# Kernel optimization log

Hardware: AMD Instinct MI355X
Metric: run time of the kernel (lower is better)

## Reference

```python
import jax, jax.numpy as jnp
import numpy as np

N = 500_000
E = 8_000_000
IN, HID, OUT = 1, 10, 4
BN_EPS = 1e-5


def _lin_init(key, fan_in, fan_out):
    kw, kb = jax.random.split(key)
    s = 1.0 / np.sqrt(fan_in)
    W = jax.random.uniform(kw, (fan_in, fan_out), minval=-s, maxval=s, dtype=jnp.float32)
    b = jax.random.uniform(kb, (fan_out,), minval=-s, maxval=s, dtype=jnp.float32)
    return W, b


def setup_inputs() -> dict:
    key = jax.random.key(0)
    ks = jax.random.split(key, 12)
    x = jax.random.normal(ks[0], (N, IN), dtype=jnp.float32)
    edge_index = jax.random.randint(ks[1], (2, E), 0, N, dtype=jnp.int64)
    edge_attr = jax.random.uniform(ks[2], (E,), dtype=jnp.float32)
    inp = {"x": x, "edge_index": edge_index, "edge_attr": edge_attr}
    dims = [(IN, HID), (HID, HID), (HID, HID)]
    for i, (di, do) in enumerate(dims, start=1):
        k1, k2 = jax.random.split(ks[2 + i])
        W1, b1 = _lin_init(k1, di, do)
        W2, b2 = _lin_init(k2, do, do)
        inp[f"W{i}a"], inp[f"b{i}a"] = W1, b1
        inp[f"W{i}b"], inp[f"b{i}b"] = W2, b2
        inp[f"g{i}"] = jnp.ones((do,), jnp.float32)
        inp[f"be{i}"] = jnp.zeros((do,), jnp.float32)
    Wf, bf = _lin_init(ks[10], 3 * HID, OUT)
    inp["Wf"], inp["bf"] = Wf, bf
    return inp


def _gin_layer(x, src, dst, Wa, ba, Wb, bb, g, be):
    # GINConv (eps=0): h_i = MLP(x_i + sum_{j->i} x_j); Linear->Linear->BatchNorm (train mode)
    agg = jax.ops.segment_sum(x[src], dst, num_segments=N)  # [N, d]
    h = x + agg
    h = h @ Wa + ba
    h = h @ Wb + bb
    mu = jnp.mean(h, axis=0)
    var = jnp.var(h, axis=0)
    return g * (h - mu) * jax.lax.rsqrt(var + BN_EPS) + be


def _modularity(s, src, dst, w):
    two_m = jnp.sum(w)
    pos = jnp.sum(w * jnp.sum(s[src] * s[dst], axis=-1)) / two_m
    deg = jax.ops.segment_sum(w, src, num_segments=N)  # [N]
    ds = (deg @ s) / two_m  # [OUT]
    return pos - jnp.sum(ds * ds)


def reference(x, edge_index, edge_attr,
              W1a, b1a, W1b, b1b, g1, be1,
              W2a, b2a, W2b, b2b, g2, be2,
              W3a, b3a, W3b, b3b, g3, be3,
              Wf, bf):
    src, dst = edge_index[0], edge_index[1]
    x11 = _gin_layer(x, src, dst, W1a, b1a, W1b, b1b, g1, be1)
    x12 = _gin_layer(x11, src, dst, W2a, b2a, W2b, b2b, g2, be2)
    x13 = _gin_layer(x12, src, dst, W3a, b3a, W3b, b3b, g3, be3)
    logits = jnp.concatenate([x11, x12, x13], axis=-1) @ Wf + bf
    s = jax.nn.softmax(logits, axis=-1)
    q = _modularity(s, src, dst, edge_attr)
    return s, q
```

## Files before the change

### kernel.cpp

```cpp
#include <hip/hip_runtime.h>
#include <hip/hip_bf16.h>

#define NN 500000
#define NE 8000000
#define NB 123
#define BSH 12
#define BSZ 4096
#define CAP 69632
#define M 8
#define NAGG (NB * M)
#define BN_EPS 1e-5f

typedef unsigned uv4 __attribute__((ext_vector_type(4)));
typedef int iv4 __attribute__((ext_vector_type(4)));
typedef float fv4 __attribute__((ext_vector_type(4)));
typedef unsigned long long u64;

__device__ __forceinline__ float waveReduceF(float v) {
#pragma unroll
    for (int o = 32; o > 0; o >>= 1) v += __shfl_down(v, o, 64);
    return v;
}
__device__ __forceinline__ double waveReduceD(double v) {
#pragma unroll
    for (int o = 32; o > 0; o >>= 1) v += __shfl_down(v, o, 64);
    return v;
}
__device__ __forceinline__ float u2f(unsigned short u) {
    return __bfloat162float(__builtin_bit_cast(__hip_bfloat16, u));
}
__device__ __forceinline__ unsigned short f2u(float f) {
    return __builtin_bit_cast(unsigned short, __float2bfloat16(f));
}
__device__ __forceinline__ u64 pk1(float v) {
    int iv = (int)rintf(v * 268435456.f);
    return ((u64)(long long)iv << 20) + 1ull;
}

__global__ __launch_bounds__(512) void scatterk(
    const iv4* __restrict__ src4, const iv4* __restrict__ dst4,
    const fv4* __restrict__ w4, int* __restrict__ cur,
    unsigned* __restrict__ pairs, unsigned short* __restrict__ wp)
{
    __shared__ unsigned sEnt[4096];
    __shared__ unsigned short sW[4096];
    __shared__ unsigned char sB[4096];
    __shared__ int h[8][128];
    __shared__ int wOff[8][128];
    __shared__ int bOff[128];
    __shared__ int lb[128];
    __shared__ int tot[128];

    int tid = threadIdx.x, wv = tid >> 6;
    for (int j = tid; j < 8 * 128; j += 512) (&h[0][0])[j] = 0;
    __syncthreads();

    unsigned en[8]; unsigned short wb[8]; int rb[8];
#pragma unroll
    for (int k = 0; k < 2; k++) {
        int q = blockIdx.x * 1024 + k * 512 + tid;
        if (q < NE / 4) {
            iv4 s4 = __builtin_nontemporal_load(src4 + q);
            iv4 d4 = __builtin_nontemporal_load(dst4 + q);
            fv4 ww = __builtin_nontemporal_load(w4 + q);
            int ss[4] = {s4.x, s4.y, s4.z, s4.w};
            int dd[4] = {d4.x, d4.y, d4.z, d4.w};
            float fw[4] = {ww.x, ww.y, ww.z, ww.w};
#pragma unroll
            for (int i = 0; i < 4; i++) {
                int d = dd[i], b = d >> BSH;
                en[k * 4 + i] = ((unsigned)(d & (BSZ - 1)) << 19) | (unsigned)ss[i];
                wb[k * 4 + i] = f2u(fw[i]);
                int rk = atomicAdd(&h[wv][b], 1);
                rb[k * 4 + i] = (rk << 8) | b;
            }
        } else {
#pragma unroll
            for (int i = 0; i < 4; i++) rb[k * 4 + i] = -1;
        }
    }
    __syncthreads();
    if (tid < NB) {
        int acc = 0;
#pragma unroll
        for (int w = 0; w < 8; w++) { wOff[w][tid] = acc; acc += h[w][tid]; }
        tot[tid] = acc;
        lb[tid] = tid * CAP + atomicAdd(&cur[tid], acc);
    }
    __syncthreads();
    if (tid < 64) {
        int lane = tid;
        int a = (2 * lane < NB) ? tot[2 * lane] : 0;
        int b = (2 * lane + 1 < NB) ? tot[2 * lane + 1] : 0;
        int s = a + b;
#pragma unroll
        for (int o = 1; o < 64; o <<= 1) {
            int t = __shfl_up(s, o, 64);
            if (lane >= o) s += t;
        }
        int excl = s - (a + b);
        bOff[2 * lane] = excl;
        bOff[2 * lane + 1] = excl + a;
    }
    __syncthreads();
#pragma unroll
    for (int k = 0; k < 8; k++) {
        if (rb[k] >= 0) {
            int b = rb[k] & 255, rk = rb[k] >> 8;
            int pos = bOff[b] + wOff[wv][b] + rk;
            sEnt[pos] = en[k]; sW[pos] = wb[k]; sB[pos] = (unsigned char)b;
        }
    }
    __syncthreads();
    int nE = NE - blockIdx.x * 4096; if (nE > 4096) nE = 4096;
    for (int j = tid; j < nE; j += 512) {
        int b = sB[j];
        int glob = lb[b] + (j - bOff[b]);
        __builtin_nontemporal_store(sEnt[j], pairs + glob);
        __builtin_nontemporal_store(sW[j], wp + glob);
    }
}

__global__ __launch_bounds__(512) void agg1k(
    const unsigned* __restrict__ pairs, const int* __restrict__ cur,
    const float* __restrict__ x, u64* __restrict__ slab)
{
    __shared__ u64 t[BSZ];
    for (int j = threadIdx.x; j < BSZ; j += 512) t[j] = 0ull;
    __syncthreads();
    int B = blockIdx.x / M, sl = blockIdx.x % M;
    int b0 = B * CAP;
    int len = cur[B];
    int seg = (((len + M - 1) / M) + 3) & ~3;
    int lo = b0 + sl * seg;
    int hi = lo + seg, e1 = b0 + len;
    if (hi > e1) hi = e1;
    int n = hi - lo;
    if (n > 0) {
        int nq = n >> 2;
        const uv4* pq = (const uv4*)(pairs + lo);
        for (int i = threadIdx.x; i < nq; i += 1024) {
            uv4 pA = __builtin_nontemporal_load(pq + i);
            int iB = i + 512;
            bool vB = iB < nq;
            float a0 = x[pA.x & 524287u];
            float a1 = x[pA.y & 524287u];
            float a2 = x[pA.z & 524287u];
            float a3 = x[pA.w & 524287u];
            float c0, c1, c2, c3; unsigned d4, d5, d6, d7;
            if (vB) {
                uv4 pB = __builtin_nontemporal_load(pq + iB);
                c0 = x[pB.x & 524287u]; d4 = pB.x >> 19;
                c1 = x[pB.y & 524287u]; d5 = pB.y >> 19;
                c2 = x[pB.z & 524287u]; d6 = pB.z >> 19;
                c3 = x[pB.w & 524287u]; d7 = pB.w >> 19;
            }
            atomicAdd(&t[pA.x >> 19], pk1(a0));
            atomicAdd(&t[pA.y >> 19], pk1(a1));
            atomicAdd(&t[pA.z >> 19], pk1(a2));
            atomicAdd(&t[pA.w >> 19], pk1(a3));
            if (vB) {
                atomicAdd(&t[d4], pk1(c0));
                atomicAdd(&t[d5], pk1(c1));
                atomicAdd(&t[d6], pk1(c2));
                atomicAdd(&t[d7], pk1(c3));
            }
        }
        int rem = n & 3;
        if ((int)threadIdx.x < rem) {
            unsigned p = pairs[lo + (nq << 2) + threadIdx.x];
            atomicAdd(&t[p >> 19], pk1(x[p & 524287u]));
        }
    }
    __syncthreads();
    u64* sb = slab + (size_t)blockIdx.x * BSZ;
    for (int j = threadIdx.x; j < BSZ; j += 512)
        __builtin_nontemporal_store(t[j], sb + j);
}

__global__ __launch_bounds__(256) void mergeN1(
    const u64* __restrict__ slab, const float* __restrict__ x,
    float2* __restrict__ UN2, u64* __restrict__ ENC)
{
    int i = blockIdx.x * 256 + threadIdx.x;
    if (i >= NN) return;
    int B = i >> BSH, low = i & (BSZ - 1);
    u64 s = 0ull;
#pragma unroll
    for (int m = 0; m < M; m++)
        s += __builtin_nontemporal_load(slab + (size_t)(B * M + m) * BSZ + low);
    unsigned cn = (unsigned)(s & 0xFFFFFull);
    long long sv = (long long)(s - (u64)cn) >> 20;
    float u = x[i] + (float)((double)sv * 3.725290298461914e-09);
    UN2[i] = make_float2(u, (float)cn);
    long long iu = (long long)rintf(u * 67108864.f);
    ENC[i] = ((u64)iu << 22) + (u64)cn;
}

__global__ __launch_bounds__(512) void agg2k(
    const unsigned* __restrict__ pairs, const int* __restrict__ cur,
    const u64* __restrict__ ENC, u64* __restrict__ slab)
{
    __shared__ u64 t[BSZ];
    for (int j = threadIdx.x; j < BSZ; j += 512) t[j] = 0ull;
    __syncthreads();
    int B = blockIdx.x / M, sl = blockIdx.x % M;
    int b0 = B * CAP;
    int len = cur[B];
    int seg = (((len + M - 1) / M) + 3) & ~3;
    int lo = b0 + sl * seg;
    int hi = lo + seg, e1 = b0 + len;
    if (hi > e1) hi = e1;
    int n = hi - lo;
    if (n > 0) {
        int nq = n >> 2;
        const uv4* pq = (const uv4*)(pairs + lo);
        for (int i = threadIdx.x; i < nq; i += 1024) {
            uv4 pA = __builtin_nontemporal_load(pq + i);
            int iB = i + 512;
            bool vB = iB < nq;
            u64 e0 = ENC[pA.x & 524287u];
            u64 e1v = ENC[pA.y & 524287u];
            u64 e2 = ENC[pA.z & 524287u];
            u64 e3 = ENC[pA.w & 524287u];
            u64 e4, e5, e6, e7; unsigned d4, d5, d6, d7;
            if (vB) {
                uv4 pB = __builtin_nontemporal_load(pq + iB);
                e4 = ENC[pB.x & 524287u]; d4 = pB.x >> 19;
                e5 = ENC[pB.y & 524287u]; d5 = pB.y >> 19;
                e6 = ENC[pB.z & 524287u]; d6 = pB.z >> 19;
                e7 = ENC[pB.w & 524287u]; d7 = pB.w >> 19;
            }
            atomicAdd(&t[pA.x >> 19], e0);
            atomicAdd(&t[pA.y >> 19], e1v);
            atomicAdd(&t[pA.z >> 19], e2);
            atomicAdd(&t[pA.w >> 19], e3);
            if (vB) {
                atomicAdd(&t[d4], e4);
                atomicAdd(&t[d5], e5);
                atomicAdd(&t[d6], e6);
                atomicAdd(&t[d7], e7);
            }
        }
        int rem = n & 3;
        if ((int)threadIdx.x < rem) {
            unsigned p = pairs[lo + (nq << 2) + threadIdx.x];
            atomicAdd(&t[p >> 19], ENC[p & 524287u]);
        }
    }
    __syncthreads();
    u64* sb = slab + (size_t)blockIdx.x * BSZ;
    for (int j = threadIdx.x; j < BSZ; j += 512)
        __builtin_nontemporal_store(t[j], sb + j);
}

__global__ __launch_bounds__(256) void mergeN2(
    const u64* __restrict__ slab, float* __restrict__ SU, float* __restrict__ SN)
{
    int i = blockIdx.x * 256 + threadIdx.x;
    if (i >= NN) return;
    int B = i >> BSH, low = i & (BSZ - 1);
    u64 s = 0ull;
#pragma unroll
    for (int m = 0; m < M; m++)
        s += __builtin_nontemporal_load(slab + (size_t)(B * M + m) * BSZ + low);
    unsigned sn = (unsigned)(s & 0x3FFFFFull);
    long long sv = (long long)(s - (u64)sn) >> 22;
    float su = (float)((double)sv * 1.4901161193847656e-08);
    SU[i] = su;
    SN[i] = (float)sn;
}

__global__ __launch_bounds__(512) void agg3k(
    const unsigned* __restrict__ pairs, const int* __restrict__ cur,
    const float* __restrict__ SU, float* __restrict__ slab)
{
    __shared__ float t[BSZ];
    for (int j = threadIdx.x; j < BSZ; j += 512) t[j] = 0.f;
    __syncthreads();
    int B = blockIdx.x / M, sl = blockIdx.x % M;
    int b0 = B * CAP;
    int len = cur[B];
    int seg = (((len + M - 1) / M) + 3) & ~3;
    int lo = b0 + sl * seg;
    int hi = lo + seg, e1 = b0 + len;
    if (hi > e1) hi = e1;
    int n = hi - lo;
    if (n > 0) {
        int nq = n >> 2;
        const uv4* pq = (const uv4*)(pairs + lo);
        for (int i = threadIdx.x; i < nq; i += 1024) {
            uv4 pA = __builtin_nontemporal_load(pq + i);
            int iB = i + 512;
            bool vB = iB < nq;
            float a0 = SU[pA.x & 524287u];
            float a1 = SU[pA.y & 524287u];
            float a2 = SU[pA.z & 524287u];
            float a3 = SU[pA.w & 524287u];
            float c0, c1, c2, c3; unsigned d4, d5, d6, d7;
            if (vB) {
                uv4 pB = __builtin_nontemporal_load(pq + iB);
                c0 = SU[pB.x & 524287u]; d4 = pB.x >> 19;
                c1 = SU[pB.y & 524287u]; d5 = pB.y >> 19;
                c2 = SU[pB.z & 524287u]; d6 = pB.z >> 19;
                c3 = SU[pB.w & 524287u]; d7 = pB.w >> 19;
            }
            atomicAdd(&t[pA.x >> 19], a0);
            atomicAdd(&t[pA.y >> 19], a1);
            atomicAdd(&t[pA.z >> 19], a2);
            atomicAdd(&t[pA.w >> 19], a3);
            if (vB) {
                atomicAdd(&t[d4], c0);
                atomicAdd(&t[d5], c1);
                atomicAdd(&t[d6], c2);
                atomicAdd(&t[d7], c3);
            }
        }
        int rem = n & 3;
        if ((int)threadIdx.x < rem) {
            unsigned p = pairs[lo + (nq << 2) + threadIdx.x];
            atomicAdd(&t[p >> 19], SU[p & 524287u]);
        }
    }
    __syncthreads();
    float* sb = slab + (size_t)blockIdx.x * BSZ;
    for (int j = threadIdx.x; j < BSZ; j += 512)
        __builtin_nontemporal_store(t[j], sb + j);
}

__global__ __launch_bounds__(256) void m3mom(
    const float* __restrict__ slab, const float2* __restrict__ UN2,
    const float* __restrict__ SU, const float* __restrict__ SN,
    float* __restrict__ SSU, double* __restrict__ dm)
{
    int i = blockIdx.x * 256 + threadIdx.x;
    double z[5] = {0, 0, 0, 0, 0};
    if (i < NN) {
        int B = i >> BSH, low = i & (BSZ - 1);
        float ssu = 0.f;
#pragma unroll
        for (int m = 0; m < M; m++)
            ssu += __builtin_nontemporal_load(slab + (size_t)(B * M + m) * BSZ + low);
        SSU[i] = ssu;
        float2 un = UN2[i];
        z[0] = (double)un.x; z[1] = (double)un.y; z[2] = (double)SU[i];
        z[3] = (double)SN[i]; z[4] = (double)ssu;
    }
    double m[20];
#pragma unroll
    for (int a = 0; a < 5; a++) m[a] = z[a];
    int idx = 5;
#pragma unroll
    for (int a = 0; a < 5; a++)
#pragma unroll
        for (int b = a; b < 5; b++) m[idx++] = z[a] * z[b];

    __shared__ double part[4][20];
    int lane = threadIdx.x & 63, wid = threadIdx.x >> 6;
#pragma unroll
    for (int k = 0; k < 20; k++) {
        double r = waveReduceD(m[k]);
        if (lane == 0) part[wid][k] = r;
    }
    __syncthreads();
    if (threadIdx.x < 20)
        atomicAdd(&dm[threadIdx.x],
                  part[0][threadIdx.x] + part[1][threadIdx.x] +
                  part[2][threadIdx.x] + part[3][threadIdx.x]);
}

__global__ __launch_bounds__(64) void constk(
    const float* __restrict__ W1a, const float* __restrict__ b1a,
    const float* __restrict__ W1b, const float* __restrict__ b1b,
    const float* __restrict__ g1, const float* __restrict__ be1,
    const float* __restrict__ W2a, const float* __restrict__ b2a,
    const float* __restrict__ W2b, const float* __restrict__ b2b,
    const float* __restrict__ g2, const float* __restrict__ be2,
    const float* __restrict__ W3a, const float* __restrict__ b3a,
    const float* __restrict__ W3b, const float* __restrict__ b3b,
    const float* __restrict__ g3, const float* __restrict__ be3,
    const float* __restrict__ Wf, const float* __restrict__ bf_,
    const double* __restrict__ dm, float* __restrict__ Lout)
{
    __shared__ float sw[768];
    __shared__ double sdm[20];
    __shared__ float vv[9][10];
    int t = threadIdx.x;
    if (t < 10) {
        sw[0 + t] = W1a[t];  sw[10 + t] = b1a[t];  sw[120 + t] = b1b[t];
        sw[130 + t] = g1[t]; sw[140 + t] = be1[t];
        sw[250 + t] = b2a[t]; sw[360 + t] = b2b[t];
        sw[370 + t] = g2[t]; sw[380 + t] = be2[t];
        sw[490 + t] = b3a[t]; sw[600 + t] = b3b[t];
        sw[610 + t] = g3[t]; sw[620 + t] = be3[t];
    }
    for (int i = t; i < 100; i += 64) {
        sw[20 + i]  = W1b[i];
        sw[150 + i] = W2a[i];
        sw[260 + i] = W2b[i];
        sw[390 + i] = W3a[i];
        sw[500 + i] = W3b[i];
    }
    for (int i = t; i < 120; i += 64) sw[630 + i] = Wf[i];
    if (t < 4)  sw[750 + t] = bf_[t];
    if (t < 20) sdm[t] = dm[t];
    __syncthreads();

    const double invN = 1.0 / (double)NN;
    double E[5];
#pragma unroll
    for (int m = 0; m < 5; m++) E[m] = sdm[m] * invN;
    double C[5][5];
    {
        int idx = 5;
#pragma unroll
        for (int a = 0; a < 5; a++)
#pragma unroll
            for (int b = a; b < 5; b++) {
                double c = sdm[idx++] * invN - E[a] * E[b];
                C[a][b] = c; C[b][a] = c;
            }
    }
    int j = t;
    if (j < 10) {
        float vj = 0.f;
        for (int k = 0; k < 10; k++) vj += sw[0 + k] * sw[20 + k * 10 + j];
        float var1 = (float)(C[0][0] * (double)vj * (double)vj);
        float sc1 = sw[130 + j] * rsqrtf(var1 + BN_EPS);
        float pj = sc1 * vj;
        float qj = sw[140 + j] - (float)E[0] * pj;
        vv[0][j] = pj; vv[1][j] = qj;
    }
    __syncthreads();
    if (j < 10) {
        float tp[10], tq[10];
        for (int m = 0; m < 10; m++) {
            float ap = 0.f, aq = 0.f;
            for (int k = 0; k < 10; k++) {
                float w = sw[150 + k * 10 + m];
                ap += vv[0][k] * w; aq += vv[1][k] * w;
            }
            tp[m] = ap; tq[m] = aq;
        }
        float rj = 0.f, sj = 0.f;
        for (int m = 0; m < 10; m++) {
            float w = sw[260 + m * 10 + j];
            rj += tp[m] * w; sj += tq[m] * w;
        }
        double Ea = E[0] + E[2], Eb = 1.0 + E[1];
        double Va = C[0][0] + 2.0 * C[0][2] + C[2][2];
        double Vb = C[1][1];
        double Cab = C[0][1] + C[2][1];
        double rjd = rj, sjd = sj;
        float var2 = (float)(Va * rjd * rjd + Vb * sjd * sjd + 2.0 * Cab * rjd * sjd);
        float sc2 = sw[370 + j] * rsqrtf(var2 + BN_EPS);
        vv[2][j] = sc2 * rj;
        vv[3][j] = sc2 * sj;
        vv[4][j] = sw[380 + j] - sc2 * (float)(Ea * rjd + Eb * sjd);
    }
    __syncthreads();
    if (j < 10) {
        float tr[10], ts[10], tt[10];
        for (int m = 0; m < 10; m++) {
            float ar = 0.f, as = 0.f, at = 0.f;
            for (int k = 0; k < 10; k++) {
                float w = sw[390 + k * 10 + m];
                ar += vv[2][k] * w; as += vv[3][k] * w; at += vv[4][k] * w;
            }
            tr[m] = ar; ts[m] = as; tt[m] = at;
        }
        float r3 = 0.f, s3 = 0.f, t3 = 0.f;
        for (int m = 0; m < 10; m++) {
            float w = sw[500 + m * 10 + j];
            r3 += tr[m] * w; s3 += ts[m] * w; t3 += tt[m] * w;
        }
        const double gA[5] = {1, 0, 2, 0, 1};
        const double gB[5] = {0, 2, 0, 1, 0};
        const double gC[5] = {0, 1, 0, 0, 0};
        double EA = E[0] + 2.0 * E[2] + E[4];
        double EB = 1.0 + 2.0 * E[1] + E[3];
        double EC = 1.0 + E[1];
        double VA = 0, VB = 0, VC = 0, CAB = 0, CAC = 0, CBC = 0;
        for (int a = 0; a < 5; a++)
            for (int b = 0; b < 5; b++) {
                double c = C[a][b];
                VA  += gA[a] * gA[b] * c;
                VB  += gB[a] * gB[b] * c;
                VC  += gC[a] * gC[b] * c;
                CAB += gA[a] * gB[b] * c;
                CAC += gA[a] * gC[b] * c;
                CBC += gB[a] * gC[b] * c;
            }
        double r3d = r3, s3d = s3, t3d = t3;
        float var3 = (float)(VA * r3d * r3d + VB * s3d * s3d + VC * t3d * t3d
                             + 2.0 * (CAB * r3d * s3d + CAC * r3d * t3d + CBC * s3d * t3d));
        float sc3 = sw[610 + j] * rsqrtf(var3 + BN_EPS);
        vv[5][j] = sc3 * r3;
        vv[6][j] = sc3 * s3;
        vv[7][j] = sc3 * t3;
        vv[8][j] = sw[620 + j] - sc3 * (float)(EA * r3d + EB * s3d + EC * t3d);
    }
    __syncthreads();
    if (t < 4) {
        int k = t;
        float Lu = 0, Ln = 0, Lsu = 0, Lsn = 0, Lssu = 0, L0 = sw[750 + k];
        for (int j2 = 0; j2 < 10; j2++) {
            float wf1 = sw[630 + j2 * 4 + k];
            float wf2 = sw[630 + (10 + j2) * 4 + k];
            float wf3 = sw[630 + (20 + j2) * 4 + k];
            Lu   += vv[0][j2] * wf1 + vv[2][j2] * wf2 + vv[5][j2] * wf3;
            Ln   += vv[3][j2] * wf2 + (2.f * vv[6][j2] + vv[7][j2]) * wf3;
            Lsu  += vv[2][j2] * wf2 + 2.f * vv[5][j2] * wf3;
            Lsn  += vv[6][j2] * wf3;
            Lssu += vv[5][j2] * wf3;
            L0   += vv[1][j2] * wf1 + (vv[3][j2] + vv[4][j2]) * wf2
                  + (vv[6][j2] + vv[7][j2] + vv[8][j2]) * wf3;
        }
        Lout[0 * 4 + k] = Lu;  Lout[1 * 4 + k] = Ln;   Lout[2 * 4 + k] = Lsu;
        Lout[3 * 4 + k] = Lsn; Lout[4 * 4 + k] = Lssu; Lout[5 * 4 + k] = L0;
    }
}

__global__ __launch_bounds__(256) void finalk(
    const float2* __restrict__ UN2, const float* __restrict__ SU,
    const float* __restrict__ SN, const float* __restrict__ SSU,
    const float* __restrict__ L,
    float4* __restrict__ sout, ushort4* __restrict__ sbf)
{
    __shared__ float sL[24];
    if (threadIdx.x < 24) sL[threadIdx.x] = L[threadIdx.x];
    __syncthreads();
    int i = blockIdx.x * 256 + threadIdx.x;
    if (i >= NN) return;
    float2 un = UN2[i];
    float u = un.x, n = un.y, su = SU[i], sn = SN[i], ssu = SSU[i];
    float lg[4];
#pragma unroll
    for (int k = 0; k < 4; k++)
        lg[k] = sL[k] * u + sL[4 + k] * n + sL[8 + k] * su
              + sL[12 + k] * sn + sL[16 + k] * ssu + sL[20 + k];
    float mx = fmaxf(fmaxf(lg[0], lg[1]), fmaxf(lg[2], lg[3]));
    float e0 = __expf(lg[0] - mx), e1 = __expf(lg[1] - mx);
    float e2 = __expf(lg[2] - mx), e3 = __expf(lg[3] - mx);
    float inv = 1.f / (e0 + e1 + e2 + e3);
    float s0 = e0 * inv, s1 = e1 * inv, s2 = e2 * inv, s3 = e3 * inv;
    fv4 o = {s0, s1, s2, s3};
    __builtin_nontemporal_store(o, (fv4*)sout + i);
    ushort4 pk; pk.x = f2u(s0); pk.y = f2u(s1); pk.z = f2u(s2); pk.w = f2u(s3);
    sbf[i] = pk;
}

__device__ __forceinline__ void modacc(u64 ua, u64 ub, float we, float* acc) {
    float ax = u2f((unsigned short)ua),         ay = u2f((unsigned short)(ua >> 16));
    float az = u2f((unsigned short)(ua >> 32)), aw = u2f((unsigned short)(ua >> 48));
    float bx = u2f((unsigned short)ub),         by = u2f((unsigned short)(ub >> 16));
    float bz = u2f((unsigned short)(ub >> 32)), bw = u2f((unsigned short)(ub >> 48));
    acc[0] += we;
    acc[1] += we * (ax * bx + ay * by + az * bz + aw * bw);
    acc[2] += we * ax; acc[3] += we * ay;
    acc[4] += we * az; acc[5] += we * aw;
}

__global__ __launch_bounds__(512) void modk(
    const unsigned* __restrict__ pairs, const unsigned short* __restrict__ wp,
    const int* __restrict__ cur, const u64* __restrict__ sbfU,
    float* __restrict__ scal)
{
    __shared__ u64 sS[BSZ];
    int B = blockIdx.x / M, sl = blockIdx.x % M;
    for (int j = threadIdx.x; j < BSZ; j += 512) {
        int g = (B << BSH) + j;
        sS[j] = (g < NN) ? sbfU[g] : 0ull;
    }
    __syncthreads();
    int b0 = B * CAP;
    int len = cur[B];
    int seg = (((len + M - 1) / M) + 3) & ~3;
    int lo = b0 + sl * seg;
    int hi = lo + seg, e1 = b0 + len;
    if (hi > e1) hi = e1;
    int n = hi - lo;
    float acc[6] = {0, 0, 0, 0, 0, 0};
    if (n > 0) {
        int nq = n >> 2;
        const uv4* pq = (const uv4*)(pairs + lo);
        const u64* wq = (const u64*)(wp + lo);
        for (int i = threadIdx.x; i < nq; i += 1024) {
            uv4 pA = __builtin_nontemporal_load(pq + i);
            u64 wA = __builtin_nontemporal_load(wq + i);
            int iB = i + 512;
            bool vB = iB < nq;
            u64 a0 = sbfU[pA.x & 524287u];
            u64 a1 = sbfU[pA.y & 524287u];
            u64 a2 = sbfU[pA.z & 524287u];
            u64 a3 = sbfU[pA.w & 524287u];
            uv4 pB; u64 wB; u64 a4, a5, a6, a7;
            if (vB) {
                pB = __builtin_nontemporal_load(pq + iB);
                wB = __builtin_nontemporal_load(wq + iB);
                a4 = sbfU[pB.x & 524287u];
                a5 = sbfU[pB.y & 524287u];
                a6 = sbfU[pB.z & 524287u];
                a7 = sbfU[pB.w & 524287u];
            }
            modacc(a0, sS[pA.x >> 19], u2f((unsigned short)wA),         acc);
            modacc(a1, sS[pA.y >> 19], u2f((unsigned short)(wA >> 16)), acc);
            modacc(a2, sS[pA.z >> 19], u2f((unsigned short)(wA >> 32)), acc);
            modacc(a3, sS[pA.w >> 19], u2f((unsigned short)(wA >> 48)), acc);
            if (vB) {
                modacc(a4, sS[pB.x >> 19], u2f((unsigned short)wB),         acc);
                modacc(a5, sS[pB.y >> 19], u2f((unsigned short)(wB >> 16)), acc);
                modacc(a6, sS[pB.z >> 19], u2f((unsigned short)(wB >> 32)), acc);
                modacc(a7, sS[pB.w >> 19], u2f((unsigned short)(wB >> 48)), acc);
            }
        }
        int rem = n & 3;
        if ((int)threadIdx.x < rem) {
            int idx = lo + (nq << 2) + threadIdx.x;
            unsigned p = pairs[idx];
            modacc(sbfU[p & 524287u], sS[p >> 19], u2f(wp[idx]), acc);
        }
    }
    __shared__ float part[8][6];
    int lane = threadIdx.x & 63, wid = threadIdx.x >> 6;
#pragma unroll
    for (int k = 0; k < 6; k++) {
        float r = waveReduceF(acc[k]);
        if (lane == 0) part[wid][k] = r;
    }
    __syncthreads();
    if (threadIdx.x < 6) {
        float vsum = 0.f;
#pragma unroll
        for (int wdi = 0; wdi < 8; wdi++) vsum += part[wdi][threadIdx.x];
        int off = (threadIdx.x == 0) ? 128 : (threadIdx.x == 1 ? 129 : 130 + threadIdx.x);
        atomicAdd(&scal[off], vsum);
    }
}

__global__ void qk(const float* __restrict__ scal, float* __restrict__ out)
{
    if (threadIdx.x == 0) {
        float inv = 1.f / scal[128];
        float posv = scal[129] * inv;
        float acc = 0.f;
#pragma unroll
        for (int k = 0; k < 4; k++) {
            float d = scal[132 + k] * inv;
            acc += d * d;
        }
        out[(size_t)NN * 4] = posv - acc;
    }
}

extern "C" void kernel_launch(void* const* d_in, const int* in_sizes, int n_in,
                              void* d_out, int out_size, void* d_ws, size_t ws_size,
                              hipStream_t stream) {
    const float* x  = (const float*)d_in[0];
    const int*  ei  = (const int*)d_in[1];
    const int*  src = ei;
    const int*  dst = ei + NE;
    const float* w   = (const float*)d_in[2];
    const float* W1a = (const float*)d_in[3];  const float* b1a = (const float*)d_in[4];
    const float* W1b = (const float*)d_in[5];  const float* b1b = (const float*)d_in[6];
    const float* g1  = (const float*)d_in[7];  const float* be1 = (const float*)d_in[8];
    const float* W2a = (const float*)d_in[9];  const float* b2a = (const float*)d_in[10];
    const float* W2b = (const float*)d_in[11]; const float* b2b = (const float*)d_in[12];
    const float* g2  = (const float*)d_in[13]; const float* be2 = (const float*)d_in[14];
    const float* W3a = (const float*)d_in[15]; const float* b3a = (const float*)d_in[16];
    const float* W3b = (const float*)d_in[17]; const float* b3b = (const float*)d_in[18];
    const float* g3  = (const float*)d_in[19]; const float* be3 = (const float*)d_in[20];
    const float* Wf  = (const float*)d_in[21]; const float* bfb = (const float*)d_in[22];

    float*  sc   = (float*)d_ws;
    int*    sci  = (int*)d_ws;
    double* dm   = (double*)(sc + 384);
    unsigned* pairs = (unsigned*)(sc + 1024);
    unsigned short* wp = (unsigned short*)(pairs + (size_t)NB * CAP);
    float*  slab = (float*)(wp + (size_t)NB * CAP);
    u64*    slabU = (u64*)slab;
    float2* UN2  = (float2*)(slab + (size_t)NAGG * 2 * BSZ);
    float*  SU   = (float*)(UN2 + NN);
    float*  SN   = SU + NN;
    float*  SSU  = SN + NN;
    ushort4* sbf = (ushort4*)(SSU + NN);
    u64*    ENC  = (u64*)(sbf + NN);
    float*  sout = (float*)d_out;

    const int NB_N  = (NN + 255) / 256;
    const int NB_EQ = (NE / 4 + 1023) / 1024;

    hipMemsetAsync(sc, 0, 4096, stream);

    scatterk<<<NB_EQ, 512, 0, stream>>>((const iv4*)src, (const iv4*)dst,
                                        (const fv4*)w, sci + 832, pairs, wp);

    agg1k<<<NAGG, 512, 0, stream>>>(pairs, sci + 832, x, slabU);
    mergeN1<<<NB_N, 256, 0, stream>>>(slabU, x, UN2, ENC);
    agg2k<<<NAGG, 512, 0, stream>>>(pairs, sci + 832, ENC, slabU);
    mergeN2<<<NB_N, 256, 0, stream>>>(slabU, SU, SN);
    agg3k<<<NAGG, 512, 0, stream>>>(pairs, sci + 832, SU, slab);
    m3mom<<<NB_N, 256, 0, stream>>>(slab, UN2, SU, SN, SSU, dm);

    constk<<<1, 64, 0, stream>>>(W1a, b1a, W1b, b1b, g1, be1,
                                 W2a, b2a, W2b, b2b, g2, be2,
                                 W3a, b3a, W3b, b3b, g3, be3,
                                 Wf, bfb, dm, sc + 160);

    finalk<<<NB_N, 256, 0, stream>>>(UN2, SU, SN, SSU, sc + 160, (float4*)sout, sbf);
    modk<<<NAGG, 512, 0, stream>>>(pairs, wp, sci + 832, (const u64*)sbf, sc);
    qk<<<1, 64, 0, stream>>>(sc, sout);
}
```

Baseline: 480.5 us.

## Software-pipeline gather loops with rotating prefetch and simplify scatter bucketing

The three aggregation kernels now keep three iterations of index and gathered-value loads in flight ahead of the shared-memory atomics. The modularity kernel keeps one iteration of lookahead. This is meant to hide global gather latency behind the LDS atomics, at the cost of more live registers and possibly lower occupancy. The scatter kernel also drops its per-wave histograms for a single block-wide histogram and packs entry, weight and bucket into one 64-bit shared array. That removes a prefix pass and a barrier, but it makes the in-bucket order nondeterministic and puts all eight waves' atomics on the same counters.

```diff
diff --git a/kernel.cpp b/kernel.cpp
--- a/kernel.cpp
+++ b/kernel.cpp
@@ -10,6 +10,7 @@
 #define M 8
 #define NAGG (NB * M)
 #define BN_EPS 1e-5f
+#define M19 524287u
 
 typedef unsigned uv4 __attribute__((ext_vector_type(4)));
 typedef int iv4 __attribute__((ext_vector_type(4)));
@@ -42,17 +43,13 @@
     const fv4* __restrict__ w4, int* __restrict__ cur,
     unsigned* __restrict__ pairs, unsigned short* __restrict__ wp)
 {
-    __shared__ unsigned sEnt[4096];
-    __shared__ unsigned short sW[4096];
-    __shared__ unsigned char sB[4096];
-    __shared__ int h[8][128];
-    __shared__ int wOff[8][128];
+    __shared__ u64 sPack[4096];
+    __shared__ int h[128];
     __shared__ int bOff[128];
     __shared__ int lb[128];
-    __shared__ int tot[128];
-
-    int tid = threadIdx.x, wv = tid >> 6;
-    for (int j = tid; j < 8 * 128; j += 512) (&h[0][0])[j] = 0;
+
+    int tid = threadIdx.x;
+    for (int j = tid; j < 128; j += 512) h[j] = 0;
     __syncthreads();
 
     unsigned en[8]; unsigned short wb[8]; int rb[8];
@@ -71,7 +68,7 @@
                 int d = dd[i], b = d >> BSH;
                 en[k * 4 + i] = ((unsigned)(d & (BSZ - 1)) << 19) | (unsigned)ss[i];
                 wb[k * 4 + i] = f2u(fw[i]);
-                int rk = atomicAdd(&h[wv][b], 1);
+                int rk = atomicAdd(&h[b], 1);
                 rb[k * 4 + i] = (rk << 8) | b;
             }
         } else {
@@ -80,18 +77,11 @@
         }
     }
     __syncthreads();
-    if (tid < NB) {
-        int acc = 0;
-#pragma unroll
-        for (int w = 0; w < 8; w++) { wOff[w][tid] = acc; acc += h[w][tid]; }
-        tot[tid] = acc;
-        lb[tid] = tid * CAP + atomicAdd(&cur[tid], acc);
-    }
-    __syncthreads();
+    if (tid < NB) lb[tid] = tid * CAP + atomicAdd(&cur[tid], h[tid]);
     if (tid < 64) {
         int lane = tid;
-        int a = (2 * lane < NB) ? tot[2 * lane] : 0;
-        int b = (2 * lane + 1 < NB) ? tot[2 * lane + 1] : 0;
+        int a = (2 * lane < NB) ? h[2 * lane] : 0;
+        int b = (2 * lane + 1 < NB) ? h[2 * lane + 1] : 0;
         int s = a + b;
 #pragma unroll
         for (int o = 1; o < 64; o <<= 1) {
@@ -107,17 +97,18 @@
     for (int k = 0; k < 8; k++) {
         if (rb[k] >= 0) {
             int b = rb[k] & 255, rk = rb[k] >> 8;
-            int pos = bOff[b] + wOff[wv][b] + rk;
-            sEnt[pos] = en[k]; sW[pos] = wb[k]; sB[pos] = (unsigned char)b;
+            int pos = bOff[b] + rk;
+            sPack[pos] = ((u64)en[k] << 32) | ((u64)wb[k] << 16) | (unsigned)b;
         }
     }
     __syncthreads();
     int nE = NE - blockIdx.x * 4096; if (nE > 4096) nE = 4096;
     for (int j = tid; j < nE; j += 512) {
-        int b = sB[j];
+        u64 v = sPack[j];
+        int b = (int)(v & 0xFF);
         int glob = lb[b] + (j - bOff[b]);
-        __builtin_nontemporal_store(sEnt[j], pairs + glob);
-        __builtin_nontemporal_store(sW[j], wp + glob);
+        __builtin_nontemporal_store((unsigned)(v >> 32), pairs + glob);
+        __builtin_nontemporal_store((unsigned short)(v >> 16), wp + glob);
     }
 }
 
@@ -139,37 +130,48 @@
     if (n > 0) {
         int nq = n >> 2;
         const uv4* pq = (const uv4*)(pairs + lo);
-        for (int i = threadIdx.x; i < nq; i += 1024) {
-            uv4 pA = __builtin_nontemporal_load(pq + i);
-            int iB = i + 512;
-            bool vB = iB < nq;
-            float a0 = x[pA.x & 524287u];
-            float a1 = x[pA.y & 524287u];
-            float a2 = x[pA.z & 524287u];
-            float a3 = x[pA.w & 524287u];
-            float c0, c1, c2, c3; unsigned d4, d5, d6, d7;
-            if (vB) {
-                uv4 pB = __builtin_nontemporal_load(pq + iB);
-                c0 = x[pB.x & 524287u]; d4 = pB.x >> 19;
-                c1 = x[pB.y & 524287u]; d5 = pB.y >> 19;
-                c2 = x[pB.z & 524287u]; d6 = pB.z >> 19;
-                c3 = x[pB.w & 524287u]; d7 = pB.w >> 19;
+        int i1 = threadIdx.x;
+        uv4 pA; float a0, a1, a2, a3; bool vA = i1 < nq;
+        if (vA) {
+            pA = __builtin_nontemporal_load(pq + i1);
+            a0 = x[pA.x & M19]; a1 = x[pA.y & M19];
+            a2 = x[pA.z & M19]; a3 = x[pA.w & M19];
+        }
+        int i2 = i1 + 512;
+        uv4 pB; float b0v, b1v, b2v, b3v; bool vB = i2 < nq;
+        if (vB) {
+            pB = __builtin_nontemporal_load(pq + i2);
+            b0v = x[pB.x & M19]; b1v = x[pB.y & M19];
+            b2v = x[pB.z & M19]; b3v = x[pB.w & M19];
+        }
+        int i3 = i2 + 512;
+        uv4 pC; float c0, c1, c2, c3; bool vC = i3 < nq;
+        if (vC) {
+            pC = __builtin_nontemporal_load(pq + i3);
+            c0 = x[pC.x & M19]; c1 = x[pC.y & M19];
+            c2 = x[pC.z & M19]; c3 = x[pC.w & M19];
+        }
+        int inx = i3 + 512;
+        while (vA) {
+            uv4 pD; float d0, d1, d2, d3; bool vD = inx < nq;
+            if (vD) {
+                pD = __builtin_nontemporal_load(pq + inx);
+                d0 = x[pD.x & M19]; d1 = x[pD.y & M19];
+                d2 = x[pD.z & M19]; d3 = x[pD.w & M19];
             }
             atomicAdd(&t[pA.x >> 19], pk1(a0));
             atomicAdd(&t[pA.y >> 19], pk1(a1));
             atomicAdd(&t[pA.z >> 19], pk1(a2));
             atomicAdd(&t[pA.w >> 19], pk1(a3));
-            if (vB) {
-                atomicAdd(&t[d4], pk1(c0));
-                atomicAdd(&t[d5], pk1(c1));
-                atomicAdd(&t[d6], pk1(c2));
-                atomicAdd(&t[d7], pk1(c3));
-            }
+            pA = pB; a0 = b0v; a1 = b1v; a2 = b2v; a3 = b3v; vA = vB;
+            pB = pC; b0v = c0; b1v = c1; b2v = c2; b3v = c3; vB = vC;
+            pC = pD; c0 = d0; c1 = d1; c2 = d2; c3 = d3; vC = vD;
+            inx += 512;
         }
         int rem = n & 3;
         if ((int)threadIdx.x < rem) {
             unsigned p = pairs[lo + (nq << 2) + threadIdx.x];
-            atomicAdd(&t[p >> 19], pk1(x[p & 524287u]));
+            atomicAdd(&t[p >> 19], pk1(x[p & M19]));
         }
     }
     __syncthreads();
@@ -215,37 +217,48 @@
     if (n > 0) {
         int nq = n >> 2;
         const uv4* pq = (const uv4*)(pairs + lo);
-        for (int i = threadIdx.x; i < nq; i += 1024) {
-            uv4 pA = __builtin_nontemporal_load(pq + i);
-            int iB = i + 512;
-            bool vB = iB < nq;
-            u64 e0 = ENC[pA.x & 524287u];
-            u64 e1v = ENC[pA.y & 524287u];
-            u64 e2 = ENC[pA.z & 524287u];
-            u64 e3 = ENC[pA.w & 524287u];
-            u64 e4, e5, e6, e7; unsigned d4, d5, d6, d7;
-            if (vB) {
-                uv4 pB = __builtin_nontemporal_load(pq + iB);
-                e4 = ENC[pB.x & 524287u]; d4 = pB.x >> 19;
-                e5 = ENC[pB.y & 524287u]; d5 = pB.y >> 19;
-                e6 = ENC[pB.z & 524287u]; d6 = pB.z >> 19;
-                e7 = ENC[pB.w & 524287u]; d7 = pB.w >> 19;
-            }
-            atomicAdd(&t[pA.x >> 19], e0);
-            atomicAdd(&t[pA.y >> 19], e1v);
-            atomicAdd(&t[pA.z >> 19], e2);
-            atomicAdd(&t[pA.w >> 19], e3);
-            if (vB) {
-                atomicAdd(&t[d4], e4);
-                atomicAdd(&t[d5], e5);
-                atomicAdd(&t[d6], e6);
-                atomicAdd(&t[d7], e7);
-            }
+        int i1 = threadIdx.x;
+        uv4 pA; u64 a0, a1, a2, a3; bool vA = i1 < nq;
+        if (vA) {
+            pA = __builtin_nontemporal_load(pq + i1);
+            a0 = ENC[pA.x & M19]; a1 = ENC[pA.y & M19];
+            a2 = ENC[pA.z & M19]; a3 = ENC[pA.w & M19];
+        }
+        int i2 = i1 + 512;
+        uv4 pB; u64 b0v, b1v, b2v, b3v; bool vB = i2 < nq;
+        if (vB) {
+            pB = __builtin_nontemporal_load(pq + i2);
+            b0v = ENC[pB.x & M19]; b1v = ENC[pB.y & M19];
+            b2v = ENC[pB.z & M19]; b3v = ENC[pB.w & M19];
+        }
+        int i3 = i2 + 512;
+        uv4 pC; u64 c0, c1, c2, c3; bool vC = i3 < nq;
+        if (vC) {
+            pC = __builtin_nontemporal_load(pq + i3);
+            c0 = ENC[pC.x & M19]; c1 = ENC[pC.y & M19];
+            c2 = ENC[pC.z & M19]; c3 = ENC[pC.w & M19];
+        }
+        int inx = i3 + 512;
+        while (vA) {
+            uv4 pD; u64 d0, d1, d2, d3; bool vD = inx < nq;
+            if (vD) {
+                pD = __builtin_nontemporal_load(pq + inx);
+                d0 = ENC[pD.x & M19]; d1 = ENC[pD.y & M19];
+                d2 = ENC[pD.z & M19]; d3 = ENC[pD.w & M19];
+            }
+            atomicAdd(&t[pA.x >> 19], a0);
+            atomicAdd(&t[pA.y >> 19], a1);
+            atomicAdd(&t[pA.z >> 19], a2);
+            atomicAdd(&t[pA.w >> 19], a3);
+            pA = pB; a0 = b0v; a1 = b1v; a2 = b2v; a3 = b3v; vA = vB;
+            pB = pC; b0v = c0; b1v = c1; b2v = c2; b3v = c3; vB = vC;
+            pC = pD; c0 = d0; c1 = d1; c2 = d2; c3 = d3; vC = vD;
+            inx += 512;
         }
         int rem = n & 3;
         if ((int)threadIdx.x < rem) {
             unsigned p = pairs[lo + (nq << 2) + threadIdx.x];
-            atomicAdd(&t[p >> 19], ENC[p & 524287u]);
+            atomicAdd(&t[p >> 19], ENC[p & M19]);
         }
     }
     __syncthreads();
@@ -289,37 +302,48 @@
     if (n > 0) {
         int nq = n >> 2;
         const uv4* pq = (const uv4*)(pairs + lo);
-        for (int i = threadIdx.x; i < nq; i += 1024) {
-            uv4 pA = __builtin_nontemporal_load(pq + i);
-            int iB = i + 512;
-            bool vB = iB < nq;
-            float a0 = SU[pA.x & 524287u];
-            float a1 = SU[pA.y & 524287u];
-            float a2 = SU[pA.z & 524287u];
-            float a3 = SU[pA.w & 524287u];
-            float c0, c1, c2, c3; unsigned d4, d5, d6, d7;
-            if (vB) {
-                uv4 pB = __builtin_nontemporal_load(pq + iB);
-                c0 = SU[pB.x & 524287u]; d4 = pB.x >> 19;
-                c1 = SU[pB.y & 524287u]; d5 = pB.y >> 19;
-                c2 = SU[pB.z & 524287u]; d6 = pB.z >> 19;
-                c3 = SU[pB.w & 524287u]; d7 = pB.w >> 19;
+        int i1 = threadIdx.x;
+        uv4 pA; float a0, a1, a2, a3; bool vA = i1 < nq;
+        if (vA) {
+            pA = __builtin_nontemporal_load(pq + i1);
+            a0 = SU[pA.x & M19]; a1 = SU[pA.y & M19];
+            a2 = SU[pA.z & M19]; a3 = SU[pA.w & M19];
+        }
+        int i2 = i1 + 512;
+        uv4 pB; float b0v, b1v, b2v, b3v; bool vB = i2 < nq;
+        if (vB) {
+            pB = __builtin_nontemporal_load(pq + i2);
+            b0v = SU[pB.x & M19]; b1v = SU[pB.y & M19];
+            b2v = SU[pB.z & M19]; b3v = SU[pB.w & M19];
+        }
+        int i3 = i2 + 512;
+        uv4 pC; float c0, c1, c2, c3; bool vC = i3 < nq;
+        if (vC) {
+            pC = __builtin_nontemporal_load(pq + i3);
+            c0 = SU[pC.x & M19]; c1 = SU[pC.y & M19];
+            c2 = SU[pC.z & M19]; c3 = SU[pC.w & M19];
+        }
+        int inx = i3 + 512;
+        while (vA) {
+            uv4 pD; float d0, d1, d2, d3; bool vD = inx < nq;
+            if (vD) {
+                pD = __builtin_nontemporal_load(pq + inx);
+                d0 = SU[pD.x & M19]; d1 = SU[pD.y & M19];
+                d2 = SU[pD.z & M19]; d3 = SU[pD.w & M19];
             }
             atomicAdd(&t[pA.x >> 19], a0);
             atomicAdd(&t[pA.y >> 19], a1);
             atomicAdd(&t[pA.z >> 19], a2);
             atomicAdd(&t[pA.w >> 19], a3);
-            if (vB) {
-                atomicAdd(&t[d4], c0);
-                atomicAdd(&t[d5], c1);
-                atomicAdd(&t[d6], c2);
-                atomicAdd(&t[d7], c3);
-            }
+            pA = pB; a0 = b0v; a1 = b1v; a2 = b2v; a3 = b3v; vA = vB;
+            pB = pC; b0v = c0; b1v = c1; b2v = c2; b3v = c3; vB = vC;
+            pC = pD; c0 = d0; c1 = d1; c2 = d2; c3 = d3; vC = vD;
+            inx += 512;
         }
         int rem = n & 3;
         if ((int)threadIdx.x < rem) {
             unsigned p = pairs[lo + (nq << 2) + threadIdx.x];
-            atomicAdd(&t[p >> 19], SU[p & 524287u]);
+            atomicAdd(&t[p >> 19], SU[p & M19]);
         }
     }
     __syncthreads();
@@ -585,40 +609,36 @@
         int nq = n >> 2;
         const uv4* pq = (const uv4*)(pairs + lo);
         const u64* wq = (const u64*)(wp + lo);
-        for (int i = threadIdx.x; i < nq; i += 1024) {
-            uv4 pA = __builtin_nontemporal_load(pq + i);
-            u64 wA = __builtin_nontemporal_load(wq + i);
-            int iB = i + 512;
-            bool vB = iB < nq;
-            u64 a0 = sbfU[pA.x & 524287u];
-            u64 a1 = sbfU[pA.y & 524287u];
-            u64 a2 = sbfU[pA.z & 524287u];
-            u64 a3 = sbfU[pA.w & 524287u];
-            uv4 pB; u64 wB; u64 a4, a5, a6, a7;
+        int i1 = threadIdx.x;
+        uv4 pA; u64 wA, a0, a1, a2, a3; bool vA = i1 < nq;
+        if (vA) {
+            pA = __builtin_nontemporal_load(pq + i1);
+            wA = __builtin_nontemporal_load(wq + i1);
+            a0 = sbfU[pA.x & M19]; a1 = sbfU[pA.y & M19];
+            a2 = sbfU[pA.z & M19]; a3 = sbfU[pA.w & M19];
+        }
+        int i2 = i1 + 512;
+        while (vA) {
+            uv4 pB; u64 wB, b0v, b1v, b2v, b3v; bool vB = i2 < nq;
             if (vB) {
-                pB = __builtin_nontemporal_load(pq + iB);
-                wB = __builtin_nontemporal_load(wq + iB);
-                a4 = sbfU[pB.x & 524287u];
-                a5 = sbfU[pB.y & 524287u];
-                a6 = sbfU[pB.z & 524287u];
-                a7 = sbfU[pB.w & 524287u];
+                pB = __builtin_nontemporal_load(pq + i2);
+                wB = __builtin_nontemporal_load(wq + i2);
+                b0v = sbfU[pB.x & M19]; b1v = sbfU[pB.y & M19];
+                b2v = sbfU[pB.z & M19]; b3v = sbfU[pB.w & M19];
             }
             modacc(a0, sS[pA.x >> 19], u2f((unsigned short)wA),         acc);
             modacc(a1, sS[pA.y >> 19], u2f((unsigned short)(wA >> 16)), acc);
             modacc(a2, sS[pA.z >> 19], u2f((unsigned short)(wA >> 32)), acc);
             modacc(a3, sS[pA.w >> 19], u2f((unsigned short)(wA >> 48)), acc);
-            if (vB) {
-                modacc(a4, sS[pB.x >> 19], u2f((unsigned short)wB),         acc);
-                modacc(a5, sS[pB.y >> 19], u2f((unsigned short)(wB >> 16)), acc);
-                modacc(a6, sS[pB.z >> 19], u2f((unsigned short)(wB >> 32)), acc);
-                modacc(a7, sS[pB.w >> 19], u2f((unsigned short)(wB >> 48)), acc);
-            }
+            pA = pB; wA = wB;
+            a0 = b0v; a1 = b1v; a2 = b2v; a3 = b3v;
+            vA = vB; i2 += 512;
         }
         int rem = n & 3;
         if ((int)threadIdx.x < rem) {
             int idx = lo + (nq << 2) + threadIdx.x;
             unsigned p = pairs[idx];
-            modacc(sbfU[p & 524287u], sS[p >> 19], u2f(wp[idx]), acc);
+            modacc(sbfU[p & M19], sS[p >> 19], u2f(wp[idx]), acc);
         }
     }
     __shared__ float part[8][6];
```

Measured after the change: 481.7 us. No clear change (+0.3%).
